# Performance work log

Hardware: AMD Instinct MI355X
Metric: run time of the kernel (lower is better)

## Reference

```python
import jax, jax.numpy as jnp
import numpy as np

D = 2048          # input_dim == dec_hidden_size
S = 16384         # src_time_steps
H = 250           # projection hidden (hard-coded in module)


def setup_inputs() -> dict:
    key = jax.random.key(0)
    ks = jax.random.split(key, 12)
    sc_d = 1.0 / np.sqrt(D)
    sc_3d = 1.0 / np.sqrt(3 * D)
    sc_h = 1.0 / np.sqrt(H)
    return {
        "s_prev": jax.random.normal(ks[0], (1, 1, D), jnp.float32),
        "enc_hs": jax.random.normal(ks[1], (1, S, D), jnp.float32),
        "cur_men_rep": jax.random.normal(ks[2], (1, 1, D), jnp.float32),
        "src_mask": jax.random.randint(ks[3], (1, S), 0, 2, jnp.int32),
        "W_info": jax.random.normal(ks[4], (D, D), jnp.float32) * sc_d,
        "W_ctx": jax.random.normal(ks[5], (D, D), jnp.float32) * sc_d,
        "W_q": jax.random.normal(ks[6], (D, D), jnp.float32) * sc_d,
        "b_q": jnp.zeros((D,), jnp.float32),
        "W_p1": jax.random.normal(ks[7], (H, 3 * D), jnp.float32) * sc_3d,
        "b_p1": jnp.zeros((H,), jnp.float32),
        "W_p2": jax.random.normal(ks[8], (1, H), jnp.float32) * sc_h,
        "b_p2": jnp.zeros((1,), jnp.float32),
    }


def reference(s_prev, enc_hs, cur_men_rep, src_mask,
              W_info, W_ctx, W_q, b_q, W_p1, b_p1, W_p2, b_p2):
    # dh = linear_info(cur_men_rep): [1,1,D]; uh = linear_ctx(enc_hs): [1,S,D]
    dh = jnp.einsum('bqe,de->bqd', cur_men_rep, W_info)
    uh = jnp.einsum('bse,de->bsd', enc_hs, W_ctx)
    wq = jnp.einsum('bqe,de->bqd', s_prev, W_q) + b_q
    # cat(uh, wq.repeat, dh.repeat) -> tanh : [1,S,3D]
    wquh = jnp.tanh(jnp.concatenate(
        [uh, jnp.broadcast_to(wq, uh.shape), jnp.broadcast_to(dh, uh.shape)],
        axis=2))
    # projection: Linear(3D,250) -> Dropout(eval: identity) -> ReLU -> Linear(250,1)
    h = jax.nn.relu(jnp.einsum('bsk,hk->bsh', wquh, W_p1) + b_p1)
    scores = (jnp.einsum('bsh,oh->bso', h, W_p2) + b_p2).squeeze()   # [S] (B=1)
    scores = jnp.where(src_mask.squeeze().astype(bool), -jnp.inf, scores)
    attn = jax.nn.softmax(scores, axis=-1)                            # [S]
    ctx = jnp.sum(enc_hs * attn[None, :, None], axis=1)               # [1,D]
    return attn, ctx
```

## Files before the change

kernel.cpp:

```cpp
#include <hip/hip_runtime.h>
#include <hip/hip_bf16.h>
#include <stdint.h>

#define DD 2048
#define SS 16384
#define HH 250

typedef __attribute__((ext_vector_type(8))) short bf16x8;
typedef __attribute__((ext_vector_type(4))) short bf16x4;
typedef __attribute__((ext_vector_type(4))) float f32x4;

__device__ __forceinline__ unsigned short f2bf(float f){
  union { float f; uint32_t u; } v; v.f = f;
  uint32_t u = v.u;
  return (unsigned short)((u + 0x7fffu + ((u >> 16) & 1u)) >> 16);
}
__device__ __forceinline__ float fast_tanh(float x){
  return 1.0f - 2.0f / (1.0f + __expf(2.0f * x));
}
__device__ __forceinline__ void gl_lds16(const void* g, void* l){
  __builtin_amdgcn_global_load_lds((const __attribute__((address_space(1))) void*)g,
                                   (__attribute__((address_space(3))) void*)l, 16, 0, 0);
}

__global__ __launch_bounds__(1024) void scan_kernel(const int* __restrict__ mask,
                                                    int* __restrict__ idx,
                                                    int* __restrict__ mcount)
{
  __shared__ int cnt[1024];
  const int t = threadIdx.x;
  const int base = t * 16;
  int loc[16];
  int c = 0;
  #pragma unroll
  for(int i = 0; i < 16; i++){ loc[i] = (mask[base + i] == 0); c += loc[i]; }
  cnt[t] = c;
  __syncthreads();
  for(int off = 1; off < 1024; off <<= 1){
    int v = (t >= off) ? cnt[t - off] : 0;
    __syncthreads();
    cnt[t] += v;
    __syncthreads();
  }
  int p = cnt[t] - c;
  #pragma unroll
  for(int i = 0; i < 16; i++) if(loc[i]) idx[p++] = base + i;
  if(t == 1023){
    int total = cnt[1023];
    mcount[0] = total;
    mcount[1] = (total + 255) & ~255;
  }
}

__global__ __launch_bounds__(256) void conv_enc_kernel(
    const float* __restrict__ enc, const int* __restrict__ idx,
    const int* __restrict__ mcount, unsigned short* __restrict__ out)
{
  const int j = blockIdx.x;
  if(j >= mcount[1]) return;
  const int t = threadIdx.x;
  unsigned short* o = out + (size_t)j * DD + t * 8;
  if(j >= mcount[0]){
    bf16x8 z;
    #pragma unroll
    for(int i = 0; i < 8; i++) z[i] = 0;
    *(bf16x8*)o = z;
    return;
  }
  const float* s = enc + (size_t)idx[j] * DD + t * 8;
  const float4* p = (const float4*)s;
  float4 a = p[0], b = p[1];
  bf16x8 v;
  v[0]=(short)f2bf(a.x); v[1]=(short)f2bf(a.y); v[2]=(short)f2bf(a.z); v[3]=(short)f2bf(a.w);
  v[4]=(short)f2bf(b.x); v[5]=(short)f2bf(b.y); v[6]=(short)f2bf(b.z); v[7]=(short)f2bf(b.w);
  *(bf16x8*)o = v;
}

__global__ void conv_wctx_kernel(const float* __restrict__ w, unsigned short* __restrict__ o){
  const int n8 = (DD * DD) / 8;
  for(int i = blockIdx.x * 256 + threadIdx.x; i < n8; i += gridDim.x * 256){
    const float4* p = (const float4*)(w + (size_t)i * 8);
    float4 a = p[0], b = p[1];
    bf16x8 v;
    v[0]=(short)f2bf(a.x); v[1]=(short)f2bf(a.y); v[2]=(short)f2bf(a.z); v[3]=(short)f2bf(a.w);
    v[4]=(short)f2bf(b.x); v[5]=(short)f2bf(b.y); v[6]=(short)f2bf(b.z); v[7]=(short)f2bf(b.w);
    *(bf16x8*)(o + (size_t)i * 8) = v;
  }
}

__global__ void conv_wp1a_kernel(const float* __restrict__ w, unsigned short* __restrict__ o){
  int g = blockIdx.x * 256 + threadIdx.x;
  int row = g >> 8, col = (g & 255) * 8;
  const float* s = w + (size_t)row * (3 * DD) + col;
  bf16x8 v;
  #pragma unroll
  for(int j = 0; j < 8; j++) v[j] = (row < HH) ? (short)f2bf(s[j]) : (short)0;
  *(bf16x8*)(o + (size_t)g * 8) = v;
}

__global__ void vec_kernel(const float* __restrict__ s_prev, const float* __restrict__ cmr,
                           const float* __restrict__ Wq, const float* __restrict__ bq,
                           const float* __restrict__ Winfo,
                           float* __restrict__ twq, float* __restrict__ tdh)
{
  int wid = threadIdx.x >> 6, lane = threadIdx.x & 63;
  bool isq = blockIdx.x < 512;
  int r = (isq ? blockIdx.x : blockIdx.x - 512) * 4 + wid;
  const float* M = (isq ? Wq : Winfo) + (size_t)r * DD;
  const float* x = isq ? s_prev : cmr;
  float s = 0.f;
  for(int i = lane; i < DD; i += 64) s += M[i] * x[i];
  #pragma unroll
  for(int o = 32; o; o >>= 1) s += __shfl_xor(s, o);
  if(lane == 0){
    if(isq) twq[r] = fast_tanh(s + bq[r]);
    else    tdh[r] = fast_tanh(s);
  }
}

__global__ void bias2_kernel(const float* __restrict__ wp1, const float* __restrict__ bp1,
                             const float* __restrict__ twq, const float* __restrict__ tdh,
                             float* __restrict__ bias2)
{
  int h = blockIdx.x * 4 + (threadIdx.x >> 6);
  int lane = threadIdx.x & 63;
  if(h >= HH){ if(lane == 0) bias2[h] = 0.f; return; }
  const float* r1 = wp1 + (size_t)h * (3 * DD) + DD;
  const float* r2 = wp1 + (size_t)h * (3 * DD) + 2 * DD;
  float s = 0.f;
  for(int i = lane; i < DD; i += 64) s += r1[i] * twq[i] + r2[i] * tdh[i];
  #pragma unroll
  for(int o = 32; o; o >>= 1) s += __shfl_xor(s, o);
  if(lane == 0) bias2[h] = s + bp1[h];
}

__device__ __forceinline__ void stage_half(const unsigned short* __restrict__ g,
                                           int grow0, int kt, char* ldsbase,
                                           int wid, int lane)
{
  const int srow = lane >> 3;
  const int c = (lane & 7) ^ srow;
  #pragma unroll
  for(int i = 0; i < 2; i++){
    int r8 = (wid * 2 + i) * 8;
    gl_lds16((const char*)(g + (size_t)(grow0 + r8 + srow) * DD + kt) + c * 16,
             ldsbase + r8 * 128);
  }
}

__global__ __launch_bounds__(512, 2) void gemmA_kernel(
    const unsigned short* __restrict__ A, const unsigned short* __restrict__ B,
    const int* __restrict__ mcount, unsigned short* __restrict__ Ct)
{
  __shared__ alignas(128) char lds[131072];
  const int tid = threadIdx.x, lane = tid & 63, wid = tid >> 6;
  const int wm = wid >> 2, wn = wid & 3;
  const int m0 = (blockIdx.x >> 3) * 256, n0 = (blockIdx.x & 7) * 256;
  if(m0 >= mcount[1]) return;
  const int frow = lane & 15, kch = lane >> 4;

  f32x4 acc[8][4] = {};

  stage_half(A, m0,        0, lds,                 wid, lane);
  stage_half(A, m0 + 128,  0, lds + 16384,         wid, lane);
  stage_half(B, n0,        0, lds + 32768,         wid, lane);
  stage_half(B, n0 + 128,  0, lds + 49152,         wid, lane);
  stage_half(B, n0,       64, lds + 65536 + 32768, wid, lane);
  stage_half(B, n0 + 128, 64, lds + 65536 + 49152, wid, lane);
  asm volatile("s_waitcnt vmcnt(4)" ::: "memory");
  __builtin_amdgcn_s_barrier();

  #pragma unroll 2
  for(int t = 0; t < 32; t++){
    const int d = t & 1;
    char* Ab = lds + d * 65536;
    char* Bb = Ab + 32768;
    char* An = lds + (d ^ 1) * 65536;
    bf16x8 bfr[4][2];
    #pragma unroll
    for(int q = 0; q < 4; q++){
      if(q == 0){
        #pragma unroll
        for(int nr = 0; nr < 4; nr++){
          int row = wn * 64 + nr * 16 + frow;
          int xo = (row & 7) << 4;
          #pragma unroll
          for(int ks = 0; ks < 2; ks++)
            bfr[nr][ks] = *(const bf16x8*)(Bb + row * 128 + (((ks * 4 + kch) * 16) ^ xo));
        }
      }
      bf16x8 afr[2][2];
      #pragma unroll
      for(int mi = 0; mi < 2; mi++){
        int row = wm * 128 + (q * 2 + mi) * 16 + frow;
        int xo = (row & 7) << 4;
        #pragma unroll
        for(int ks = 0; ks < 2; ks++)
          afr[mi][ks] = *(const bf16x8*)(Ab + row * 128 + (((ks * 4 + kch) * 16) ^ xo));
      }
      if(q == 0){
        if(t + 1 < 32){
          stage_half(A, m0,       (t + 1) * 64, An,         wid, lane);
          stage_half(A, m0 + 128, (t + 1) * 64, An + 16384, wid, lane);
        }
      } else if(q == 1){
        if(t + 2 < 32) stage_half(B, n0,       (t + 2) * 64, Bb,         wid, lane);
      } else if(q == 2){
        if(t + 2 < 32) stage_half(B, n0 + 128, (t + 2) * 64, Bb + 16384, wid, lane);
      }
      __builtin_amdgcn_s_barrier();
      __builtin_amdgcn_sched_barrier(0);
      __builtin_amdgcn_s_setprio(1);
      #pragma unroll
      for(int mi = 0; mi < 2; mi++)
        #pragma unroll
        for(int nr = 0; nr < 4; nr++)
          #pragma unroll
          for(int ks = 0; ks < 2; ks++)
            acc[q * 2 + mi][nr] = __builtin_amdgcn_mfma_f32_16x16x32_bf16(
                afr[mi][ks], bfr[nr][ks], acc[q * 2 + mi][nr], 0, 0, 0);
      __builtin_amdgcn_s_setprio(0);
      __builtin_amdgcn_sched_barrier(0);
      if(q == 3){
        if(t < 30)       asm volatile("s_waitcnt vmcnt(4)" ::: "memory");
        else if(t == 30) asm volatile("s_waitcnt vmcnt(0)" ::: "memory");
      }
      __builtin_amdgcn_s_barrier();
    }
  }

  const int r0 = m0 + wm * 128 + (lane >> 4) * 4;
  const int c0 = n0 + wn * 64 + frow;
  #pragma unroll
  for(int mr = 0; mr < 8; mr++)
    #pragma unroll
    for(int nr = 0; nr < 4; nr++)
      #pragma unroll
      for(int r = 0; r < 4; r++)
        Ct[(size_t)(r0 + mr * 16 + r) * DD + c0 + nr * 16] = f2bf(fast_tanh(acc[mr][nr][r]));
}

__global__ __launch_bounds__(256) void gemmB_kernel(
    const unsigned short* __restrict__ A, const unsigned short* __restrict__ B,
    const int* __restrict__ mcount, const float* __restrict__ bias2,
    const float* __restrict__ w2, const float* __restrict__ bp2,
    float* __restrict__ scores)
{
  __shared__ unsigned short At[64 * 64];
  __shared__ unsigned short Bt[256 * 64];
  __shared__ float sred[4][64];
  const int tid = threadIdx.x, lane = tid & 63, w = tid >> 6;
  const int m0 = blockIdx.x * 64;
  if(m0 >= mcount[1]) return;
  const int srow = lane >> 3;
  const int scol = ((lane & 7) ^ srow) * 16;
  const int xorv = (lane & 7) << 4;
  f32x4 acc[4][4] = {};
  for(int kt = 0; kt < DD; kt += 64){
    __syncthreads();
    #pragma unroll
    for(int i = 0; i < 2; i++){
      int r8 = (w * 2 + i) * 8;
      gl_lds16((const char*)(A + (size_t)(m0 + r8 + srow) * DD + kt) + scol,
               (char*)At + r8 * 128);
    }
    #pragma unroll
    for(int i = 0; i < 8; i++){
      int r8 = (w * 8 + i) * 8;
      gl_lds16((const char*)(B + (size_t)(r8 + srow) * DD + kt) + scol,
               (char*)Bt + r8 * 128);
    }
    __syncthreads();
    #pragma unroll
    for(int ks = 0; ks < 2; ks++){
      const int cb = (ks * 4 + (lane >> 4)) * 16;
      bf16x8 af[4], bv[4];
      #pragma unroll
      for(int i = 0; i < 4; i++){
        af[i] = *(const bf16x8*)((const char*)At + (i * 16 + (lane & 15)) * 128 + (cb ^ xorv));
        bv[i] = *(const bf16x8*)((const char*)Bt + (w * 64 + i * 16 + (lane & 15)) * 128 + (cb ^ xorv));
      }
      #pragma unroll
      for(int i = 0; i < 4; i++)
        #pragma unroll
        for(int j = 0; j < 4; j++)
          acc[i][j] = __builtin_amdgcn_mfma_f32_16x16x32_bf16(af[i], bv[j], acc[i][j], 0, 0, 0);
    }
  }
  float w2v[4], b2v[4];
  #pragma unroll
  for(int in = 0; in < 4; in++){
    int n = w * 64 + in * 16 + (lane & 15);
    w2v[in] = (n < HH) ? w2[n] : 0.f;
    b2v[in] = bias2[n];
  }
  #pragma unroll
  for(int im = 0; im < 4; im++){
    #pragma unroll
    for(int r = 0; r < 4; r++){
      float s = 0.f;
      #pragma unroll
      for(int in = 0; in < 4; in++){
        float h = acc[im][in][r] + b2v[in];
        s += (h > 0.f ? h : 0.f) * w2v[in];
      }
      s += __shfl_xor(s, 1); s += __shfl_xor(s, 2);
      s += __shfl_xor(s, 4); s += __shfl_xor(s, 8);
      if((lane & 15) == 0) sred[w][im * 16 + (lane >> 4) * 4 + r] = s;
    }
  }
  __syncthreads();
  if(tid < 64)
    scores[m0 + tid] = sred[0][tid] + sred[1][tid] + sred[2][tid] + sred[3][tid] + bp2[0];
}

__global__ void scatter_kernel(const float* __restrict__ sc, const int* __restrict__ idx,
                               const int* __restrict__ mcount, float* __restrict__ sf)
{
  int j = blockIdx.x * 256 + threadIdx.x;
  if(j < mcount[0]) sf[idx[j]] = sc[j];
}

__global__ __launch_bounds__(1024) void softmax_kernel(
    const float* __restrict__ scores, const int* __restrict__ mask, float* __restrict__ attn)
{
  __shared__ float red[16];
  const int tid = threadIdx.x;
  float m = -3.0e38f;
  for(int i = tid; i < SS; i += 1024) if(mask[i] == 0) m = fmaxf(m, scores[i]);
  #pragma unroll
  for(int o = 32; o; o >>= 1) m = fmaxf(m, __shfl_xor(m, o));
  if((tid & 63) == 0) red[tid >> 6] = m;
  __syncthreads();
  float M = -3.0e38f;
  #pragma unroll
  for(int i = 0; i < 16; i++) M = fmaxf(M, red[i]);
  __syncthreads();
  float s = 0.f;
  for(int i = tid; i < SS; i += 1024) if(mask[i] == 0) s += __expf(scores[i] - M);
  #pragma unroll
  for(int o = 32; o; o >>= 1) s += __shfl_xor(s, o);
  if((tid & 63) == 0) red[tid >> 6] = s;
  __syncthreads();
  float T = 0.f;
  #pragma unroll
  for(int i = 0; i < 16; i++) T += red[i];
  const float inv = 1.0f / T;
  for(int i = tid; i < SS; i += 1024)
    attn[i] = (mask[i] == 0) ? __expf(scores[i] - M) * inv : 0.f;
}

__global__ __launch_bounds__(256) void ctxp_kernel(
    const float* __restrict__ attn, const float* __restrict__ enc, float* __restrict__ part)
{
  const int b = blockIdx.x, t = threadIdx.x;
  float a0=0,a1=0,a2=0,a3=0,a4=0,a5=0,a6=0,a7=0;
  const float* base = enc + (size_t)b * 32 * DD + t * 8;
  const float* ap = attn + b * 32;
  for(int s = 0; s < 32; s++){
    float av = ap[s];
    if(av != 0.f){
      const float4* p = (const float4*)(base + (size_t)s * DD);
      float4 x = p[0], y = p[1];
      a0 += av * x.x; a1 += av * x.y; a2 += av * x.z; a3 += av * x.w;
      a4 += av * y.x; a5 += av * y.y; a6 += av * y.z; a7 += av * y.w;
    }
  }
  float* o = part + (size_t)b * DD + t * 8;
  o[0]=a0; o[1]=a1; o[2]=a2; o[3]=a3; o[4]=a4; o[5]=a5; o[6]=a6; o[7]=a7;
}

__global__ void ctxr_kernel(const float* __restrict__ part, float* __restrict__ out){
  const int d = blockIdx.x * 256 + threadIdx.x;
  float s = 0.f;
  for(int b = 0; b < 512; b++) s += part[(size_t)b * DD + d];
  out[d] = s;
}

extern "C" void kernel_launch(void* const* d_in, const int* in_sizes, int n_in,
                              void* d_out, int out_size, void* d_ws, size_t ws_size,
                              hipStream_t stream)
{
  const float* s_prev = (const float*)d_in[0];
  const float* enc    = (const float*)d_in[1];
  const float* cmr    = (const float*)d_in[2];
  const int*   mask   = (const int*)d_in[3];
  const float* W_info = (const float*)d_in[4];
  const float* W_ctx  = (const float*)d_in[5];
  const float* W_q    = (const float*)d_in[6];
  const float* b_q    = (const float*)d_in[7];
  const float* W_p1   = (const float*)d_in[8];
  const float* b_p1   = (const float*)d_in[9];
  const float* W_p2   = (const float*)d_in[10];
  const float* b_p2   = (const float*)d_in[11];
  float* out = (float*)d_out;

  char* ws = (char*)d_ws;
  unsigned short* encb    = (unsigned short*)(ws);
  unsigned short* tanhbuf = (unsigned short*)(ws + 67108864);
  unsigned short* wctxb   = (unsigned short*)(ws + 134217728);
  unsigned short* wp1ab   = (unsigned short*)(ws + 142606336);
  int*   idx     = (int*)(ws + 143654912);
  float* scoresc = (float*)(ws + 143720448);
  float* scoresf = (float*)(ws + 143785984);
  float* twq     = (float*)(ws + 143851520);
  float* tdh     = (float*)(ws + 143859712);
  float* bias2   = (float*)(ws + 143867904);
  int*   mcount  = (int*)(ws + 143868928);
  float* part    = (float*)(ws);

  scan_kernel<<<1, 1024, 0, stream>>>(mask, idx, mcount);
  conv_enc_kernel<<<16384, 256, 0, stream>>>(enc, idx, mcount, encb);
  conv_wctx_kernel<<<512, 256, 0, stream>>>(W_ctx, wctxb);
  conv_wp1a_kernel<<<256, 256, 0, stream>>>(W_p1, wp1ab);
  vec_kernel<<<1024, 256, 0, stream>>>(s_prev, cmr, W_q, b_q, W_info, twq, tdh);
  bias2_kernel<<<64, 256, 0, stream>>>(W_p1, b_p1, twq, tdh, bias2);
  gemmA_kernel<<<512, 512, 0, stream>>>(encb, wctxb, mcount, tanhbuf);
  gemmB_kernel<<<256, 256, 0, stream>>>(tanhbuf, wp1ab, mcount, bias2, W_p2, b_p2, scoresc);
  scatter_kernel<<<64, 256, 0, stream>>>(scoresc, idx, mcount, scoresf);
  softmax_kernel<<<1, 1024, 0, stream>>>(scoresf, mask, out);
  ctxp_kernel<<<512, 256, 0, stream>>>(out, enc, part);
  ctxr_kernel<<<8, 256, 0, stream>>>(part, out + SS);
}
```

Before: 222.1 us.

## Merge prep kernels, retile GEMM-A to 288 rows, fold softmax into GEMM-B

```diff
diff --git a/kernel.cpp b/kernel.cpp
--- a/kernel.cpp
+++ b/kernel.cpp
@@ -5,9 +5,10 @@
 #define DD 2048
 #define SS 16384
 #define HH 250
+#define BMA 288
+#define GEMMB_GRID 264
 
 typedef __attribute__((ext_vector_type(8))) short bf16x8;
-typedef __attribute__((ext_vector_type(4))) short bf16x4;
 typedef __attribute__((ext_vector_type(4))) float f32x4;
 
 __device__ __forceinline__ unsigned short f2bf(float f){
@@ -15,6 +16,9 @@
   uint32_t u = v.u;
   return (unsigned short)((u + 0x7fffu + ((u >> 16) & 1u)) >> 16);
 }
+__device__ __forceinline__ float bf2f(unsigned short h){
+  union { uint32_t u; float f; } v; v.u = ((uint32_t)h) << 16; return v.f;
+}
 __device__ __forceinline__ float fast_tanh(float x){
   return 1.0f - 2.0f / (1.0f + __expf(2.0f * x));
 }
@@ -23,205 +27,210 @@
                                    (__attribute__((address_space(3))) void*)l, 16, 0, 0);
 }
 
-__global__ __launch_bounds__(1024) void scan_kernel(const int* __restrict__ mask,
-                                                    int* __restrict__ idx,
-                                                    int* __restrict__ mcount)
-{
-  __shared__ int cnt[1024];
-  const int t = threadIdx.x;
-  const int base = t * 16;
-  int loc[16];
-  int c = 0;
-  #pragma unroll
-  for(int i = 0; i < 16; i++){ loc[i] = (mask[base + i] == 0); c += loc[i]; }
-  cnt[t] = c;
-  __syncthreads();
-  for(int off = 1; off < 1024; off <<= 1){
-    int v = (t >= off) ? cnt[t - off] : 0;
+__global__ __launch_bounds__(256) void mega_kernel(
+    const float* __restrict__ W_ctx, unsigned short* __restrict__ wctxb,
+    const float* __restrict__ W_p1, unsigned short* __restrict__ wp1ab,
+    const float* __restrict__ s_prev, const float* __restrict__ cmr,
+    const float* __restrict__ Wq, const float* __restrict__ bq,
+    const float* __restrict__ Winfo,
+    float* __restrict__ twq, float* __restrict__ tdh,
+    const int* __restrict__ mask, int* __restrict__ idx, int* __restrict__ cpos,
+    int* __restrict__ mcount)
+{
+  const int b = blockIdx.x, t = threadIdx.x;
+  if(b < 512){
+    for(int i = b * 256 + t; i < (DD * DD) / 8; i += 512 * 256){
+      const float4* p = (const float4*)(W_ctx + (size_t)i * 8);
+      float4 a = p[0], c = p[1];
+      bf16x8 v;
+      v[0]=(short)f2bf(a.x); v[1]=(short)f2bf(a.y); v[2]=(short)f2bf(a.z); v[3]=(short)f2bf(a.w);
+      v[4]=(short)f2bf(c.x); v[5]=(short)f2bf(c.y); v[6]=(short)f2bf(c.z); v[7]=(short)f2bf(c.w);
+      *(bf16x8*)(wctxb + (size_t)i * 8) = v;
+    }
+  } else if(b < 768){
+    int g = (b - 512) * 256 + t;
+    int row = g >> 8, col = (g & 255) * 8;
+    const float* s = W_p1 + (size_t)row * (3 * DD) + col;
+    bf16x8 v;
+    #pragma unroll
+    for(int j = 0; j < 8; j++) v[j] = (row < HH) ? (short)f2bf(s[j]) : (short)0;
+    *(bf16x8*)(wp1ab + (size_t)g * 8) = v;
+  } else if(b < 1792){
+    int vb = b - 768;
+    int wid = t >> 6, lane = t & 63;
+    bool isq = vb < 512;
+    int r = (isq ? vb : vb - 512) * 4 + wid;
+    const float* M = (isq ? Wq : Winfo) + (size_t)r * DD;
+    const float* x = isq ? s_prev : cmr;
+    float s = 0.f;
+    for(int i = lane; i < DD; i += 64) s += M[i] * x[i];
+    #pragma unroll
+    for(int o = 32; o; o >>= 1) s += __shfl_xor(s, o);
+    if(lane == 0){
+      if(isq) twq[r] = fast_tanh(s + bq[r]);
+      else    tdh[r] = fast_tanh(s);
+    }
+  } else {
+    __shared__ int cnt[256];
+    const int base = t * 64;
+    int c = 0;
+    for(int i = 0; i < 64; i++) c += (mask[base + i] == 0);
+    cnt[t] = c;
     __syncthreads();
-    cnt[t] += v;
-    __syncthreads();
-  }
-  int p = cnt[t] - c;
-  #pragma unroll
-  for(int i = 0; i < 16; i++) if(loc[i]) idx[p++] = base + i;
-  if(t == 1023){
-    int total = cnt[1023];
-    mcount[0] = total;
-    mcount[1] = (total + 255) & ~255;
+    for(int off = 1; off < 256; off <<= 1){
+      int v = (t >= off) ? cnt[t - off] : 0;
+      __syncthreads();
+      cnt[t] += v;
+      __syncthreads();
+    }
+    int p = cnt[t] - c;
+    for(int i = 0; i < 64; i++){
+      int fi = base + i;
+      if(mask[fi] == 0){ idx[p] = fi; cpos[fi] = p; p++; }
+      else cpos[fi] = -1;
+    }
+    if(t == 255){
+      int tot = cnt[255];
+      mcount[0] = tot;
+      mcount[1] = ((tot + BMA - 1) / BMA) * BMA;
+      mcount[2] = (tot + 63) & ~63;
+    }
   }
 }
 
 __global__ __launch_bounds__(256) void conv_enc_kernel(
     const float* __restrict__ enc, const int* __restrict__ idx,
-    const int* __restrict__ mcount, unsigned short* __restrict__ out)
-{
-  const int j = blockIdx.x;
-  if(j >= mcount[1]) return;
-  const int t = threadIdx.x;
-  unsigned short* o = out + (size_t)j * DD + t * 8;
-  if(j >= mcount[0]){
-    bf16x8 z;
-    #pragma unroll
-    for(int i = 0; i < 8; i++) z[i] = 0;
-    *(bf16x8*)o = z;
-    return;
-  }
-  const float* s = enc + (size_t)idx[j] * DD + t * 8;
-  const float4* p = (const float4*)s;
-  float4 a = p[0], b = p[1];
-  bf16x8 v;
-  v[0]=(short)f2bf(a.x); v[1]=(short)f2bf(a.y); v[2]=(short)f2bf(a.z); v[3]=(short)f2bf(a.w);
-  v[4]=(short)f2bf(b.x); v[5]=(short)f2bf(b.y); v[6]=(short)f2bf(b.z); v[7]=(short)f2bf(b.w);
-  *(bf16x8*)o = v;
-}
-
-__global__ void conv_wctx_kernel(const float* __restrict__ w, unsigned short* __restrict__ o){
-  const int n8 = (DD * DD) / 8;
-  for(int i = blockIdx.x * 256 + threadIdx.x; i < n8; i += gridDim.x * 256){
-    const float4* p = (const float4*)(w + (size_t)i * 8);
-    float4 a = p[0], b = p[1];
-    bf16x8 v;
-    v[0]=(short)f2bf(a.x); v[1]=(short)f2bf(a.y); v[2]=(short)f2bf(a.z); v[3]=(short)f2bf(a.w);
-    v[4]=(short)f2bf(b.x); v[5]=(short)f2bf(b.y); v[6]=(short)f2bf(b.z); v[7]=(short)f2bf(b.w);
-    *(bf16x8*)(o + (size_t)i * 8) = v;
-  }
-}
-
-__global__ void conv_wp1a_kernel(const float* __restrict__ w, unsigned short* __restrict__ o){
-  int g = blockIdx.x * 256 + threadIdx.x;
-  int row = g >> 8, col = (g & 255) * 8;
-  const float* s = w + (size_t)row * (3 * DD) + col;
-  bf16x8 v;
-  #pragma unroll
-  for(int j = 0; j < 8; j++) v[j] = (row < HH) ? (short)f2bf(s[j]) : (short)0;
-  *(bf16x8*)(o + (size_t)g * 8) = v;
-}
-
-__global__ void vec_kernel(const float* __restrict__ s_prev, const float* __restrict__ cmr,
-                           const float* __restrict__ Wq, const float* __restrict__ bq,
-                           const float* __restrict__ Winfo,
-                           float* __restrict__ twq, float* __restrict__ tdh)
-{
-  int wid = threadIdx.x >> 6, lane = threadIdx.x & 63;
-  bool isq = blockIdx.x < 512;
-  int r = (isq ? blockIdx.x : blockIdx.x - 512) * 4 + wid;
-  const float* M = (isq ? Wq : Winfo) + (size_t)r * DD;
-  const float* x = isq ? s_prev : cmr;
-  float s = 0.f;
-  for(int i = lane; i < DD; i += 64) s += M[i] * x[i];
-  #pragma unroll
-  for(int o = 32; o; o >>= 1) s += __shfl_xor(s, o);
-  if(lane == 0){
-    if(isq) twq[r] = fast_tanh(s + bq[r]);
-    else    tdh[r] = fast_tanh(s);
-  }
-}
-
-__global__ void bias2_kernel(const float* __restrict__ wp1, const float* __restrict__ bp1,
-                             const float* __restrict__ twq, const float* __restrict__ tdh,
-                             float* __restrict__ bias2)
-{
-  int h = blockIdx.x * 4 + (threadIdx.x >> 6);
-  int lane = threadIdx.x & 63;
-  if(h >= HH){ if(lane == 0) bias2[h] = 0.f; return; }
-  const float* r1 = wp1 + (size_t)h * (3 * DD) + DD;
-  const float* r2 = wp1 + (size_t)h * (3 * DD) + 2 * DD;
-  float s = 0.f;
-  for(int i = lane; i < DD; i += 64) s += r1[i] * twq[i] + r2[i] * tdh[i];
-  #pragma unroll
-  for(int o = 32; o; o >>= 1) s += __shfl_xor(s, o);
-  if(lane == 0) bias2[h] = s + bp1[h];
-}
-
-__device__ __forceinline__ void stage_half(const unsigned short* __restrict__ g,
-                                           int grow0, int kt, char* ldsbase,
+    const int* __restrict__ mcount, unsigned short* __restrict__ out,
+    const float* __restrict__ wp1, const float* __restrict__ bp1,
+    const float* __restrict__ twq, const float* __restrict__ tdh,
+    float* __restrict__ bias2)
+{
+  const int b = blockIdx.x, t = threadIdx.x;
+  if(b < 2056){
+    const int mc0 = mcount[0], mc1 = mcount[1];
+    #pragma unroll
+    for(int r = 0; r < 8; r++){
+      int j = b * 8 + r;
+      if(j >= mc1) return;
+      unsigned short* o = out + (size_t)j * DD + t * 8;
+      if(j >= mc0){
+        bf16x8 z;
+        #pragma unroll
+        for(int i = 0; i < 8; i++) z[i] = 0;
+        *(bf16x8*)o = z;
+      } else {
+        const float4* p = (const float4*)(enc + (size_t)idx[j] * DD + t * 8);
+        float4 a = p[0], c = p[1];
+        bf16x8 v;
+        v[0]=(short)f2bf(a.x); v[1]=(short)f2bf(a.y); v[2]=(short)f2bf(a.z); v[3]=(short)f2bf(a.w);
+        v[4]=(short)f2bf(c.x); v[5]=(short)f2bf(c.y); v[6]=(short)f2bf(c.z); v[7]=(short)f2bf(c.w);
+        *(bf16x8*)o = v;
+      }
+    }
+  } else {
+    int h = (b - 2056) * 4 + (t >> 6);
+    int lane = t & 63;
+    if(h >= HH){ if(lane == 0) bias2[h] = 0.f; return; }
+    const float* r1 = wp1 + (size_t)h * (3 * DD) + DD;
+    const float* r2 = wp1 + (size_t)h * (3 * DD) + 2 * DD;
+    float s = 0.f;
+    for(int i = lane; i < DD; i += 64) s += r1[i] * twq[i] + r2[i] * tdh[i];
+    #pragma unroll
+    for(int o = 32; o; o >>= 1) s += __shfl_xor(s, o);
+    if(lane == 0) bias2[h] = s + bp1[h];
+  }
+}
+
+__device__ __forceinline__ void stageA288(const unsigned short* __restrict__ g,
+                                          int grow0, int kt, char* dst, int wid, int lane)
+{
+  const int srow = lane >> 3, sc = ((lane & 7) ^ srow) * 8;
+  #pragma unroll
+  for(int i = 0; i < 5; i++){
+    int l = wid + 8 * i;
+    if(l < 36)
+      gl_lds16(g + (size_t)(grow0 + l * 8 + srow) * DD + kt + sc, dst + l * 1024);
+  }
+}
+__device__ __forceinline__ void stageBhalf(const unsigned short* __restrict__ g,
+                                           int grow0, int kt, char* dst, int half,
                                            int wid, int lane)
 {
-  const int srow = lane >> 3;
-  const int c = (lane & 7) ^ srow;
+  const int srow = lane >> 3, sc = ((lane & 7) ^ srow) * 8;
   #pragma unroll
   for(int i = 0; i < 2; i++){
-    int r8 = (wid * 2 + i) * 8;
-    gl_lds16((const char*)(g + (size_t)(grow0 + r8 + srow) * DD + kt) + c * 16,
-             ldsbase + r8 * 128);
-  }
-}
+    int l = half * 16 + wid + 8 * i;
+    gl_lds16(g + (size_t)(grow0 + l * 8 + srow) * DD + kt + sc, dst + l * 1024);
+  }
+}
+#define RDF(base, lr, kc) (*(const bf16x8*)((base) + (lr) * 128 + (((kc) * 16) ^ (((lr) & 7) << 4))))
 
 __global__ __launch_bounds__(512, 2) void gemmA_kernel(
     const unsigned short* __restrict__ A, const unsigned short* __restrict__ B,
     const int* __restrict__ mcount, unsigned short* __restrict__ Ct)
 {
-  __shared__ alignas(128) char lds[131072];
+  __shared__ alignas(128) char lds[139264];
   const int tid = threadIdx.x, lane = tid & 63, wid = tid >> 6;
   const int wm = wid >> 2, wn = wid & 3;
-  const int m0 = (blockIdx.x >> 3) * 256, n0 = (blockIdx.x & 7) * 256;
+  const int m0 = (blockIdx.x >> 3) * BMA, n0 = (blockIdx.x & 7) * 256;
   if(m0 >= mcount[1]) return;
   const int frow = lane & 15, kch = lane >> 4;
 
-  f32x4 acc[8][4] = {};
-
-  stage_half(A, m0,        0, lds,                 wid, lane);
-  stage_half(A, m0 + 128,  0, lds + 16384,         wid, lane);
-  stage_half(B, n0,        0, lds + 32768,         wid, lane);
-  stage_half(B, n0 + 128,  0, lds + 49152,         wid, lane);
-  stage_half(B, n0,       64, lds + 65536 + 32768, wid, lane);
-  stage_half(B, n0 + 128, 64, lds + 65536 + 49152, wid, lane);
+  f32x4 acc[9][4] = {};
+
+  stageA288(A, m0, 0, lds, wid, lane);
+  stageBhalf(B, n0, 0, lds + 73728, 0, wid, lane);
+  stageBhalf(B, n0, 0, lds + 73728, 1, wid, lane);
+  stageBhalf(B, n0, 64, lds + 106496, 0, wid, lane);
+  stageBhalf(B, n0, 64, lds + 106496, 1, wid, lane);
   asm volatile("s_waitcnt vmcnt(4)" ::: "memory");
   __builtin_amdgcn_s_barrier();
 
   #pragma unroll 2
   for(int t = 0; t < 32; t++){
     const int d = t & 1;
-    char* Ab = lds + d * 65536;
-    char* Bb = Ab + 32768;
-    char* An = lds + (d ^ 1) * 65536;
+    char* Ab = lds + d * 36864;
+    char* An = lds + (d ^ 1) * 36864;
+    char* Bb = lds + 73728 + d * 32768;
     bf16x8 bfr[4][2];
     #pragma unroll
-    for(int q = 0; q < 4; q++){
+    for(int q = 0; q < 3; q++){
       if(q == 0){
         #pragma unroll
         for(int nr = 0; nr < 4; nr++){
           int row = wn * 64 + nr * 16 + frow;
-          int xo = (row & 7) << 4;
           #pragma unroll
-          for(int ks = 0; ks < 2; ks++)
-            bfr[nr][ks] = *(const bf16x8*)(Bb + row * 128 + (((ks * 4 + kch) * 16) ^ xo));
+          for(int ks = 0; ks < 2; ks++) bfr[nr][ks] = RDF(Bb, row, ks * 4 + kch);
         }
       }
-      bf16x8 afr[2][2];
+      bf16x8 afr[3][2];
       #pragma unroll
-      for(int mi = 0; mi < 2; mi++){
-        int row = wm * 128 + (q * 2 + mi) * 16 + frow;
-        int xo = (row & 7) << 4;
-        #pragma unroll
-        for(int ks = 0; ks < 2; ks++)
-          afr[mi][ks] = *(const bf16x8*)(Ab + row * 128 + (((ks * 4 + kch) * 16) ^ xo));
+      for(int mi = 0; mi < 3; mi++){
+        int row = wm * 144 + (q * 3 + mi) * 16 + frow;
+        #pragma unroll
+        for(int ks = 0; ks < 2; ks++) afr[mi][ks] = RDF(Ab, row, ks * 4 + kch);
       }
       if(q == 0){
-        if(t + 1 < 32){
-          stage_half(A, m0,       (t + 1) * 64, An,         wid, lane);
-          stage_half(A, m0 + 128, (t + 1) * 64, An + 16384, wid, lane);
-        }
+        if(t + 1 < 32) stageA288(A, m0, (t + 1) * 64, An, wid, lane);
       } else if(q == 1){
-        if(t + 2 < 32) stage_half(B, n0,       (t + 2) * 64, Bb,         wid, lane);
-      } else if(q == 2){
-        if(t + 2 < 32) stage_half(B, n0 + 128, (t + 2) * 64, Bb + 16384, wid, lane);
+        if(t + 2 < 32) stageBhalf(B, n0, (t + 2) * 64, Bb, 0, wid, lane);
+      } else {
+        if(t + 2 < 32) stageBhalf(B, n0, (t + 2) * 64, Bb, 1, wid, lane);
       }
       __builtin_amdgcn_s_barrier();
       __builtin_amdgcn_sched_barrier(0);
       __builtin_amdgcn_s_setprio(1);
       #pragma unroll
-      for(int mi = 0; mi < 2; mi++)
+      for(int mi = 0; mi < 3; mi++)
         #pragma unroll
         for(int nr = 0; nr < 4; nr++)
           #pragma unroll
           for(int ks = 0; ks < 2; ks++)
-            acc[q * 2 + mi][nr] = __builtin_amdgcn_mfma_f32_16x16x32_bf16(
-                afr[mi][ks], bfr[nr][ks], acc[q * 2 + mi][nr], 0, 0, 0);
+            acc[q * 3 + mi][nr] = __builtin_amdgcn_mfma_f32_16x16x32_bf16(
+                afr[mi][ks], bfr[nr][ks], acc[q * 3 + mi][nr], 0, 0, 0);
       __builtin_amdgcn_s_setprio(0);
       __builtin_amdgcn_sched_barrier(0);
-      if(q == 3){
+      if(q == 2){
         if(t < 30)       asm volatile("s_waitcnt vmcnt(4)" ::: "memory");
         else if(t == 30) asm volatile("s_waitcnt vmcnt(0)" ::: "memory");
       }
@@ -229,10 +238,10 @@
     }
   }
 
-  const int r0 = m0 + wm * 128 + (lane >> 4) * 4;
+  const int r0 = m0 + wm * 144 + (lane >> 4) * 4;
   const int c0 = n0 + wn * 64 + frow;
   #pragma unroll
-  for(int mr = 0; mr < 8; mr++)
+  for(int mr = 0; mr < 9; mr++)
     #pragma unroll
     for(int nr = 0; nr < 4; nr++)
       #pragma unroll
@@ -240,141 +249,174 @@
         Ct[(size_t)(r0 + mr * 16 + r) * DD + c0 + nr * 16] = f2bf(fast_tanh(acc[mr][nr][r]));
 }
 
-__global__ __launch_bounds__(256) void gemmB_kernel(
+__global__ __launch_bounds__(512, 4) void gemmB_kernel(
     const unsigned short* __restrict__ A, const unsigned short* __restrict__ B,
     const int* __restrict__ mcount, const float* __restrict__ bias2,
     const float* __restrict__ w2, const float* __restrict__ bp2,
-    float* __restrict__ scores)
-{
-  __shared__ unsigned short At[64 * 64];
-  __shared__ unsigned short Bt[256 * 64];
-  __shared__ float sred[4][64];
-  const int tid = threadIdx.x, lane = tid & 63, w = tid >> 6;
+    float* __restrict__ attnc, float* __restrict__ Tpart)
+{
+  __shared__ alignas(128) char lds[81920];
+  __shared__ float sred[8][32];
+  const int tid = threadIdx.x, lane = tid & 63, wid = tid >> 6;
+  const int wm = wid >> 2, wn = wid & 3;
   const int m0 = blockIdx.x * 64;
-  if(m0 >= mcount[1]) return;
-  const int srow = lane >> 3;
-  const int scol = ((lane & 7) ^ srow) * 16;
-  const int xorv = (lane & 7) << 4;
-  f32x4 acc[4][4] = {};
-  for(int kt = 0; kt < DD; kt += 64){
-    __syncthreads();
-    #pragma unroll
-    for(int i = 0; i < 2; i++){
-      int r8 = (w * 2 + i) * 8;
-      gl_lds16((const char*)(A + (size_t)(m0 + r8 + srow) * DD + kt) + scol,
-               (char*)At + r8 * 128);
-    }
-    #pragma unroll
-    for(int i = 0; i < 8; i++){
-      int r8 = (w * 8 + i) * 8;
-      gl_lds16((const char*)(B + (size_t)(r8 + srow) * DD + kt) + scol,
-               (char*)Bt + r8 * 128);
-    }
-    __syncthreads();
-    #pragma unroll
-    for(int ks = 0; ks < 2; ks++){
-      const int cb = (ks * 4 + (lane >> 4)) * 16;
-      bf16x8 af[4], bv[4];
+  const int mc0 = mcount[0], mc2 = mcount[2];
+  if(m0 >= mc2){ if(tid == 0) Tpart[blockIdx.x] = 0.f; return; }
+  const int frow = lane & 15, kch = lane >> 4;
+  const int srow = lane >> 3, sc = ((lane & 7) ^ srow) * 8;
+
+  f32x4 acc[2][4] = {};
+
+  gl_lds16(A + (size_t)(m0 + wid * 8 + srow) * DD + sc, lds + wid * 1024);
+  #pragma unroll
+  for(int i = 0; i < 4; i++){
+    int l = wid + 8 * i;
+    gl_lds16(B + (size_t)(l * 8 + srow) * DD + sc,      lds + 16384 + l * 1024);
+    gl_lds16(B + (size_t)(l * 8 + srow) * DD + 64 + sc, lds + 49152 + l * 1024);
+  }
+  asm volatile("s_waitcnt vmcnt(4)" ::: "memory");
+  __builtin_amdgcn_s_barrier();
+
+  #pragma unroll 2
+  for(int t = 0; t < 32; t++){
+    const int d = t & 1;
+    char* Ab = lds + d * 8192;
+    char* An = lds + (d ^ 1) * 8192;
+    char* Bb = lds + 16384 + d * 32768;
+    bf16x8 bfr[4][2], afr[2];
+    #pragma unroll
+    for(int q = 0; q < 2; q++){
+      if(q == 0){
+        #pragma unroll
+        for(int nr = 0; nr < 4; nr++){
+          int row = wn * 64 + nr * 16 + frow;
+          #pragma unroll
+          for(int ks = 0; ks < 2; ks++) bfr[nr][ks] = RDF(Bb, row, ks * 4 + kch);
+        }
+      }
+      {
+        int row = wm * 32 + q * 16 + frow;
+        #pragma unroll
+        for(int ks = 0; ks < 2; ks++) afr[ks] = RDF(Ab, row, ks * 4 + kch);
+      }
+      if(q == 0){
+        if(t + 1 < 32)
+          gl_lds16(A + (size_t)(m0 + wid * 8 + srow) * DD + (t + 1) * 64 + sc, An + wid * 1024);
+      } else {
+        if(t + 2 < 32){
+          #pragma unroll
+          for(int i = 0; i < 4; i++){
+            int l = wid + 8 * i;
+            gl_lds16(B + (size_t)(l * 8 + srow) * DD + (t + 2) * 64 + sc, Bb + l * 1024);
+          }
+        }
+      }
+      __builtin_amdgcn_s_barrier();
+      __builtin_amdgcn_sched_barrier(0);
+      __builtin_amdgcn_s_setprio(1);
       #pragma unroll
-      for(int i = 0; i < 4; i++){
-        af[i] = *(const bf16x8*)((const char*)At + (i * 16 + (lane & 15)) * 128 + (cb ^ xorv));
-        bv[i] = *(const bf16x8*)((const char*)Bt + (w * 64 + i * 16 + (lane & 15)) * 128 + (cb ^ xorv));
-      }
-      #pragma unroll
-      for(int i = 0; i < 4; i++)
-        #pragma unroll
-        for(int j = 0; j < 4; j++)
-          acc[i][j] = __builtin_amdgcn_mfma_f32_16x16x32_bf16(af[i], bv[j], acc[i][j], 0, 0, 0);
-    }
-  }
+      for(int nr = 0; nr < 4; nr++)
+        #pragma unroll
+        for(int ks = 0; ks < 2; ks++)
+          acc[q][nr] = __builtin_amdgcn_mfma_f32_16x16x32_bf16(afr[ks], bfr[nr][ks], acc[q][nr], 0, 0, 0);
+      __builtin_amdgcn_s_setprio(0);
+      __builtin_amdgcn_sched_barrier(0);
+      if(q == 1){
+        if(t < 30)       asm volatile("s_waitcnt vmcnt(4)" ::: "memory");
+        else if(t == 30) asm volatile("s_waitcnt vmcnt(0)" ::: "memory");
+      }
+      __builtin_amdgcn_s_barrier();
+    }
+  }
+
   float w2v[4], b2v[4];
   #pragma unroll
   for(int in = 0; in < 4; in++){
-    int n = w * 64 + in * 16 + (lane & 15);
+    int n = wn * 64 + in * 16 + frow;
     w2v[in] = (n < HH) ? w2[n] : 0.f;
     b2v[in] = bias2[n];
   }
   #pragma unroll
-  for(int im = 0; im < 4; im++){
+  for(int mi = 0; mi < 2; mi++){
     #pragma unroll
     for(int r = 0; r < 4; r++){
       float s = 0.f;
       #pragma unroll
       for(int in = 0; in < 4; in++){
-        float h = acc[im][in][r] + b2v[in];
+        float h = acc[mi][in][r] + b2v[in];
         s += (h > 0.f ? h : 0.f) * w2v[in];
       }
       s += __shfl_xor(s, 1); s += __shfl_xor(s, 2);
       s += __shfl_xor(s, 4); s += __shfl_xor(s, 8);
-      if((lane & 15) == 0) sred[w][im * 16 + (lane >> 4) * 4 + r] = s;
+      if(frow == 0) sred[wid][mi * 16 + (lane >> 4) * 4 + r] = s;
     }
   }
   __syncthreads();
-  if(tid < 64)
-    scores[m0 + tid] = sred[0][tid] + sred[1][tid] + sred[2][tid] + sred[3][tid] + bp2[0];
-}
-
-__global__ void scatter_kernel(const float* __restrict__ sc, const int* __restrict__ idx,
-                               const int* __restrict__ mcount, float* __restrict__ sf)
-{
-  int j = blockIdx.x * 256 + threadIdx.x;
-  if(j < mcount[0]) sf[idx[j]] = sc[j];
-}
-
-__global__ __launch_bounds__(1024) void softmax_kernel(
-    const float* __restrict__ scores, const int* __restrict__ mask, float* __restrict__ attn)
-{
-  __shared__ float red[16];
-  const int tid = threadIdx.x;
-  float m = -3.0e38f;
-  for(int i = tid; i < SS; i += 1024) if(mask[i] == 0) m = fmaxf(m, scores[i]);
-  #pragma unroll
-  for(int o = 32; o; o >>= 1) m = fmaxf(m, __shfl_xor(m, o));
-  if((tid & 63) == 0) red[tid >> 6] = m;
+  if(tid < 64){
+    int wmr = tid >> 5, rr = tid & 31;
+    float s = sred[wmr * 4][rr] + sred[wmr * 4 + 1][rr] + sred[wmr * 4 + 2][rr]
+            + sred[wmr * 4 + 3][rr] + bp2[0];
+    int j = m0 + tid;
+    float e = (j < mc0) ? __expf(s) : 0.f;
+    if(j < mc0) attnc[j] = e;
+    #pragma unroll
+    for(int o = 32; o; o >>= 1) e += __shfl_xor(e, o);
+    if(tid == 0) Tpart[blockIdx.x] = e;
+  }
+}
+
+__global__ __launch_bounds__(256) void norm_kernel(
+    const float* __restrict__ attnc, const int* __restrict__ cpos,
+    const float* __restrict__ Tpart, float* __restrict__ out)
+{
+  __shared__ float sT;
+  if(threadIdx.x == 0){
+    float s = 0.f;
+    for(int i = 0; i < GEMMB_GRID; i++) s += Tpart[i];
+    sT = 1.0f / s;
+  }
   __syncthreads();
-  float M = -3.0e38f;
-  #pragma unroll
-  for(int i = 0; i < 16; i++) M = fmaxf(M, red[i]);
+  int i = blockIdx.x * 256 + threadIdx.x;
+  int cp = cpos[i];
+  out[i] = (cp >= 0) ? attnc[cp] * sT : 0.f;
+}
+
+__global__ __launch_bounds__(256) void ctxp_kernel(
+    const float* __restrict__ attnc, const unsigned short* __restrict__ encb,
+    const int* __restrict__ mcount, float* __restrict__ part)
+{
+  const int b = blockIdx.x, t = threadIdx.x;
+  const int mc0 = mcount[0];
+  const int chunk = (mc0 + 255) >> 8;
+  const int j0 = b * chunk;
+  const int j1 = min(j0 + chunk, mc0);
+  float a[8] = {};
+  for(int j = j0; j < j1; j++){
+    float e = attnc[j];
+    bf16x8 v = *(const bf16x8*)(encb + (size_t)j * DD + t * 8);
+    #pragma unroll
+    for(int k = 0; k < 8; k++) a[k] += e * bf2f((unsigned short)v[k]);
+  }
+  float* o = part + (size_t)b * DD + t * 8;
+  #pragma unroll
+  for(int k = 0; k < 8; k++) o[k] = a[k];
+}
+
+__global__ __launch_bounds__(256) void ctxr_kernel(
+    const float* __restrict__ part, const float* __restrict__ Tpart,
+    float* __restrict__ out)
+{
+  __shared__ float sT;
+  if(threadIdx.x == 0){
+    float s = 0.f;
+    for(int i = 0; i < GEMMB_GRID; i++) s += Tpart[i];
+    sT = 1.0f / s;
+  }
   __syncthreads();
+  const int dcol = blockIdx.x * 256 + threadIdx.x;
   float s = 0.f;
-  for(int i = tid; i < SS; i += 1024) if(mask[i] == 0) s += __expf(scores[i] - M);
-  #pragma unroll
-  for(int o = 32; o; o >>= 1) s += __shfl_xor(s, o);
-  if((tid & 63) == 0) red[tid >> 6] = s;
-  __syncthreads();
-  float T = 0.f;
-  #pragma unroll
-  for(int i = 0; i < 16; i++) T += red[i];
-  const float inv = 1.0f / T;
-  for(int i = tid; i < SS; i += 1024)
-    attn[i] = (mask[i] == 0) ? __expf(scores[i] - M) * inv : 0.f;
-}
-
-__global__ __launch_bounds__(256) void ctxp_kernel(
-    const float* __restrict__ attn, const float* __restrict__ enc, float* __restrict__ part)
-{
-  const int b = blockIdx.x, t = threadIdx.x;
-  float a0=0,a1=0,a2=0,a3=0,a4=0,a5=0,a6=0,a7=0;
-  const float* base = enc + (size_t)b * 32 * DD + t * 8;
-  const float* ap = attn + b * 32;
-  for(int s = 0; s < 32; s++){
-    float av = ap[s];
-    if(av != 0.f){
-      const float4* p = (const float4*)(base + (size_t)s * DD);
-      float4 x = p[0], y = p[1];
-      a0 += av * x.x; a1 += av * x.y; a2 += av * x.z; a3 += av * x.w;
-      a4 += av * y.x; a5 += av * y.y; a6 += av * y.z; a7 += av * y.w;
-    }
-  }
-  float* o = part + (size_t)b * DD + t * 8;
-  o[0]=a0; o[1]=a1; o[2]=a2; o[3]=a3; o[4]=a4; o[5]=a5; o[6]=a6; o[7]=a7;
-}
-
-__global__ void ctxr_kernel(const float* __restrict__ part, float* __restrict__ out){
-  const int d = blockIdx.x * 256 + threadIdx.x;
-  float s = 0.f;
-  for(int b = 0; b < 512; b++) s += part[(size_t)b * DD + d];
-  out[d] = s;
+  for(int b = 0; b < 256; b++) s += part[(size_t)b * DD + dcol];
+  out[dcol] = s * sT;
 }
 
 extern "C" void kernel_launch(void* const* d_in, const int* in_sizes, int n_in,
@@ -397,28 +439,28 @@
 
   char* ws = (char*)d_ws;
   unsigned short* encb    = (unsigned short*)(ws);
-  unsigned short* tanhbuf = (unsigned short*)(ws + 67108864);
-  unsigned short* wctxb   = (unsigned short*)(ws + 134217728);
-  unsigned short* wp1ab   = (unsigned short*)(ws + 142606336);
-  int*   idx     = (int*)(ws + 143654912);
-  float* scoresc = (float*)(ws + 143720448);
-  float* scoresf = (float*)(ws + 143785984);
-  float* twq     = (float*)(ws + 143851520);
-  float* tdh     = (float*)(ws + 143859712);
-  float* bias2   = (float*)(ws + 143867904);
-  int*   mcount  = (int*)(ws + 143868928);
-  float* part    = (float*)(ws);
-
-  scan_kernel<<<1, 1024, 0, stream>>>(mask, idx, mcount);
-  conv_enc_kernel<<<16384, 256, 0, stream>>>(enc, idx, mcount, encb);
-  conv_wctx_kernel<<<512, 256, 0, stream>>>(W_ctx, wctxb);
-  conv_wp1a_kernel<<<256, 256, 0, stream>>>(W_p1, wp1ab);
-  vec_kernel<<<1024, 256, 0, stream>>>(s_prev, cmr, W_q, b_q, W_info, twq, tdh);
-  bias2_kernel<<<64, 256, 0, stream>>>(W_p1, b_p1, twq, tdh, bias2);
-  gemmA_kernel<<<512, 512, 0, stream>>>(encb, wctxb, mcount, tanhbuf);
-  gemmB_kernel<<<256, 256, 0, stream>>>(tanhbuf, wp1ab, mcount, bias2, W_p2, b_p2, scoresc);
-  scatter_kernel<<<64, 256, 0, stream>>>(scoresc, idx, mcount, scoresf);
-  softmax_kernel<<<1, 1024, 0, stream>>>(scoresf, mask, out);
-  ctxp_kernel<<<512, 256, 0, stream>>>(out, enc, part);
-  ctxr_kernel<<<8, 256, 0, stream>>>(part, out + SS);
-}
+  unsigned short* tanhbuf = (unsigned short*)(ws + 67239936);
+  unsigned short* wctxb   = (unsigned short*)(ws + 134479872);
+  unsigned short* wp1ab   = (unsigned short*)(ws + 142868480);
+  int*   idx    = (int*)(ws + 143917056);
+  int*   cpos   = (int*)(ws + 143982592);
+  float* attnc  = (float*)(ws + 144048128);
+  float* part   = (float*)(ws + 144113664);
+  float* twq    = (float*)(ws + 146210816);
+  float* tdh    = (float*)(ws + 146219008);
+  float* bias2  = (float*)(ws + 146227200);
+  int*   mcount = (int*)(ws + 146228224);
+  float* Tpart  = (float*)(ws + 146228352);
+
+  mega_kernel<<<1793, 256, 0, stream>>>(W_ctx, wctxb, W_p1, wp1ab,
+                                        s_prev, cmr, W_q, b_q, W_info,
+                                        twq, tdh, mask, idx, cpos, mcount);
+  conv_enc_kernel<<<2120, 256, 0, stream>>>(enc, idx, mcount, encb,
+                                            W_p1, b_p1, twq, tdh, bias2);
+  gemmA_kernel<<<456, 512, 0, stream>>>(encb, wctxb, mcount, tanhbuf);
+  gemmB_kernel<<<GEMMB_GRID, 512, 0, stream>>>(tanhbuf, wp1ab, mcount, bias2,
+                                               W_p2, b_p2, attnc, Tpart);
+  norm_kernel<<<64, 256, 0, stream>>>(attnc, cpos, Tpart, out);
+  ctxp_kernel<<<256, 256, 0, stream>>>(attnc, encb, mcount, part);
+  ctxr_kernel<<<8, 256, 0, stream>>>(part, Tpart, out + SS);
+}
```

Measured after the change: 231.7 us. 1.04x slower.
